# Performance work log

Hardware: AMD Instinct MI355X
Metric: run time of the kernel (lower is better)

## Reference

```python
import jax, jax.numpy as jnp
import numpy as np

SIGMA_BOOST = 2.0   # sparse-hyper util.SIGMA_BOOST
EPSILON = 1e-6      # sparse-hyper util.EPSILON (10e-7)
B, N = 512, 16384   # batch, size


def setup_inputs() -> dict:
    key = jax.random.key(0)
    k1, k2, k3, k4, k5 = jax.random.split(key, 5)
    return {
        "x": jax.random.normal(k1, (B, N), jnp.float32),
        "noise": jax.random.normal(k2, (B, N, 2), jnp.float32),
        "pmeans": jax.random.normal(k3, (N, 2), jnp.float32),
        "psigmas": jax.random.normal(k4, (N,), jnp.float32),
        "pvalues": jax.random.normal(k5, (N,), jnp.float32),
    }


def reference(x, noise, pmeans, psigmas, pvalues):
    b, n = x.shape
    s = jnp.float32(n)  # square size (n, n); both dims equal
    # hyper(): transform_means = sigmoid * (size-1); transform_sigmas = (softplus(.+boost)+eps) * size
    means = jax.nn.sigmoid(pmeans)[None] * (s - 1.0)                    # (1, n, 2) -> bcast (b, n, 2)
    sigmas = (jax.nn.softplus(psigmas + SIGMA_BOOST) + EPSILON)[None, :, None] * s  # (1, n, 1)
    # Normal(means, sigmas).sample() -- non-differentiable sample
    samples = jax.lax.stop_gradient(means + sigmas * noise)             # (b, n, 2)
    # round, clamp to [0, n-1]
    indices = jnp.clip(jnp.round(samples).astype(jnp.int32), 0, n - 1)  # (b, n, 2)
    rows, cols = indices[..., 0], indices[..., 1]                       # (b, n) each
    values = jnp.broadcast_to(pvalues[None, :], (b, n))
    # sparse.contract: y[b, rows[b,t]] += values[b,t] * x[b, cols[b,t]]
    contrib = values * jnp.take_along_axis(x, cols, axis=1)             # (b, n)
    y = jnp.zeros((b, n), x.dtype).at[jnp.arange(b)[:, None], rows].add(contrib)
    return y
```

## Files before the change

kernel.cpp:

```cpp
#include <hip/hip_runtime.h>
#include <math.h>

#define SIGMA_BOOST 2.0f
#define EPSILON 1e-6f

typedef float vfloat4 __attribute__((ext_vector_type(4)));

#define PIN4(v)  asm volatile("" : "+v"(v))
#define PIN1(v)  asm volatile("" : "+v"(v))

__global__ void params_kernel(const float2* __restrict__ pmeans,
                              const float* __restrict__ psigmas,
                              const float* __restrict__ pvalues,
                              float4* __restrict__ params, int N) {
    int t = blockIdx.x * blockDim.x + threadIdx.x;
    if (t >= N) return;
    float2 pm = pmeans[t];
    float scale = (float)(N - 1);
    float m0 = __fmul_rn(__fdiv_rn(1.0f, __fadd_rn(1.0f, expf(-pm.x))), scale);
    float m1 = __fmul_rn(__fdiv_rn(1.0f, __fadd_rn(1.0f, expf(-pm.y))), scale);
    float z  = __fadd_rn(psigmas[t], SIGMA_BOOST);
    float sp = __fadd_rn(fmaxf(z, 0.0f), log1pf(expf(-fabsf(z))));
    float sg = __fmul_rn(__fadd_rn(sp, EPSILON), (float)N);
    params[t] = make_float4(m0, m1, sg, pvalues[t]);
}

template <bool INLINE_PARAMS>
__launch_bounds__(1024, 8)
__global__ void contract_kernel(const float* __restrict__ x,
                                const float2* __restrict__ noise,
                                const float4* __restrict__ params,
                                const float2* __restrict__ pmeans,
                                const float* __restrict__ psigmas,
                                const float* __restrict__ pvalues,
                                float* __restrict__ y, int N) {
    extern __shared__ float ly[];
    const int b = blockIdx.x;
    const int tid = threadIdx.x;
    const int nthr = blockDim.x;

    float4* ly4 = (float4*)ly;
    const int n4 = N >> 2;
    for (int i = tid; i < n4; i += nthr) ly4[i] = make_float4(0.f, 0.f, 0.f, 0.f);
    __syncthreads();

    const float* xb = x + (size_t)b * N;
    const float fN1 = (float)(N - 1);
    const int iN1 = N - 1;
    float acc0 = 0.0f, accE = 0.0f;

    const int steps = ((N >> 1) % nthr == 0) ? (N >> 1) / nthr : 0;

    if (!INLINE_PARAMS && steps >= 2) {
        const vfloat4* nb4 = (const vfloat4*)(noise + (size_t)b * N);
        const vfloat4* pp  = (const vfloat4*)params;

        int q = tid;
        vfloat4 nz = __builtin_nontemporal_load(&nb4[q]);
        vfloat4 pa = pp[2 * q];
        vfloat4 pb = pp[2 * q + 1];
        PIN4(nz); PIN4(pa); PIN4(pb);

        for (int s = 0; s < steps; ++s) {
            float s0 = __fadd_rn(pa.x, __fmul_rn(pa.z, nz.x));
            float s1 = __fadd_rn(pa.y, __fmul_rn(pa.z, nz.y));
            float s2 = __fadd_rn(pb.x, __fmul_rn(pb.z, nz.z));
            float s3 = __fadd_rn(pb.y, __fmul_rn(pb.z, nz.w));
            int r0 = (int)fminf(fmaxf(rintf(s0), 0.0f), fN1);
            int c0 = (int)fminf(fmaxf(rintf(s1), 0.0f), fN1);
            int r1 = (int)fminf(fmaxf(rintf(s2), 0.0f), fN1);
            int c1 = (int)fminf(fmaxf(rintf(s3), 0.0f), fN1);
            float w0 = pa.w, w1 = pb.w;
            float xv0 = xb[c0];
            float xv1 = xb[c1];
            PIN1(xv0); PIN1(xv1);

            vfloat4 nzn, pan, pbn;
            bool have_next = (s + 1 < steps);
            if (have_next) {
                int qn = q + nthr;
                nzn = __builtin_nontemporal_load(&nb4[qn]);
                pan = pp[2 * qn];
                pbn = pp[2 * qn + 1];
                PIN4(nzn); PIN4(pan); PIN4(pbn);
                q = qn;
            }

            float ctr0 = __fmul_rn(w0, xv0);
            float ctr1 = __fmul_rn(w1, xv1);
            bool lo0 = (r0 == 0), hi0 = (r0 == iN1);
            bool lo1 = (r1 == 0), hi1 = (r1 == iN1);
            if (!(lo0 | hi0)) atomicAdd(&ly[r0], ctr0);
            if (!(lo1 | hi1)) atomicAdd(&ly[r1], ctr1);
            acc0 = __fadd_rn(acc0, lo0 ? ctr0 : 0.0f);
            accE = __fadd_rn(accE, hi0 ? ctr0 : 0.0f);
            acc0 = __fadd_rn(acc0, lo1 ? ctr1 : 0.0f);
            accE = __fadd_rn(accE, hi1 ? ctr1 : 0.0f);

            if (have_next) { nz = nzn; pa = pan; pb = pbn; }
        }
    } else {
        const float2* nb = noise + (size_t)b * N;
        for (int t = tid; t < N; t += nthr) {
            float4 p;
            if (INLINE_PARAMS) {
                float2 pm = pmeans[t];
                float scale = (float)(N - 1);
                p.x = __fmul_rn(__fdiv_rn(1.0f, __fadd_rn(1.0f, expf(-pm.x))), scale);
                p.y = __fmul_rn(__fdiv_rn(1.0f, __fadd_rn(1.0f, expf(-pm.y))), scale);
                float z  = __fadd_rn(psigmas[t], SIGMA_BOOST);
                float sp = __fadd_rn(fmaxf(z, 0.0f), log1pf(expf(-fabsf(z))));
                p.z = __fmul_rn(__fadd_rn(sp, EPSILON), (float)N);
                p.w = pvalues[t];
            } else {
                p = params[t];
            }
            float2 nz = nb[t];
            float s0 = __fadd_rn(p.x, __fmul_rn(p.z, nz.x));
            float s1 = __fadd_rn(p.y, __fmul_rn(p.z, nz.y));
            int row = (int)fminf(fmaxf(rintf(s0), 0.0f), fN1);
            int col = (int)fminf(fmaxf(rintf(s1), 0.0f), fN1);
            float xv = xb[col];
            float ctr = __fmul_rn(p.w, xv);
            bool lo = (row == 0);
            bool hi = (row == iN1);
            if (!(lo | hi)) atomicAdd(&ly[row], ctr);
            acc0 = __fadd_rn(acc0, lo ? ctr : 0.0f);
            accE = __fadd_rn(accE, hi ? ctr : 0.0f);
        }
    }

    for (int off = 32; off > 0; off >>= 1) {
        acc0 = __fadd_rn(acc0, __shfl_down(acc0, off, 64));
        accE = __fadd_rn(accE, __shfl_down(accE, off, 64));
    }
    if ((tid & 63) == 0) {
        atomicAdd(&ly[0], acc0);
        atomicAdd(&ly[iN1], accE);
    }
    __syncthreads();

    const vfloat4* lv4 = (const vfloat4*)ly;
    vfloat4* yb4 = (vfloat4*)(y + (size_t)b * N);
    for (int i = tid; i < n4; i += nthr)
        __builtin_nontemporal_store(lv4[i], &yb4[i]);
}

extern "C" void kernel_launch(void* const* d_in, const int* in_sizes, int n_in,
                              void* d_out, int out_size, void* d_ws, size_t ws_size,
                              hipStream_t stream) {
    const float*  x       = (const float*)d_in[0];
    const float2* noise   = (const float2*)d_in[1];
    const float2* pmeans  = (const float2*)d_in[2];
    const float*  psigmas = (const float*)d_in[3];
    const float*  pvalues = (const float*)d_in[4];
    float* y = (float*)d_out;

    const int N = in_sizes[3];
    const int B = in_sizes[0] / N;

    const size_t params_bytes = (size_t)N * sizeof(float4);
    const bool use_ws = (ws_size >= params_bytes) && (d_ws != nullptr);

    const int block = 1024;
    const size_t lds_bytes = (size_t)N * sizeof(float);

    if (use_ws) {
        float4* params = (float4*)d_ws;
        params_kernel<<<(N + 255) / 256, 256, 0, stream>>>(pmeans, psigmas,
                                                           pvalues, params, N);
        contract_kernel<false><<<B, block, lds_bytes, stream>>>(
            x, noise, params, nullptr, nullptr, nullptr, y, N);
    } else {
        contract_kernel<true><<<B, block, lds_bytes, stream>>>(
            x, noise, nullptr, pmeans, psigmas, pvalues, y, N);
    }
}
```

Measured before the change: 149.2 us.

## Stage each batch row of x in LDS and gather from shared memory

Each block now loads its full row of x into a second LDS buffer with coalesced vec4 loads while zeroing the accumulator, then does the random column gather from LDS instead of global memory. This targets the uncoalesced, cache-unfriendly global gathers. In exchange it doubles LDS per block to 128KB, which cuts resident blocks per CU (the launch-bounds hint is lowered to match), and adds a serial staging phase before compute. The kernel decides on the fast path from the shape alone, not from whether the larger LDS allocation actually succeeded, so a failed attribute call would read past its shared memory.

```diff
diff --git a/kernel.cpp b/kernel.cpp
--- a/kernel.cpp
+++ b/kernel.cpp
@@ -7,7 +7,6 @@
 typedef float vfloat4 __attribute__((ext_vector_type(4)));
 
 #define PIN4(v)  asm volatile("" : "+v"(v))
-#define PIN1(v)  asm volatile("" : "+v"(v))
 
 __global__ void params_kernel(const float2* __restrict__ pmeans,
                               const float* __restrict__ psigmas,
@@ -26,7 +25,7 @@
 }
 
 template <bool INLINE_PARAMS>
-__launch_bounds__(1024, 8)
+__launch_bounds__(1024, 4)
 __global__ void contract_kernel(const float* __restrict__ x,
                                 const float2* __restrict__ noise,
                                 const float4* __restrict__ params,
@@ -34,24 +33,38 @@
                                 const float* __restrict__ psigmas,
                                 const float* __restrict__ pvalues,
                                 float* __restrict__ y, int N) {
-    extern __shared__ float ly[];
+    extern __shared__ float lds[];
+    float* ly = lds;
+    float* lx = lds + N;
     const int b = blockIdx.x;
     const int tid = threadIdx.x;
     const int nthr = blockDim.x;
 
-    float4* ly4 = (float4*)ly;
-    const int n4 = N >> 2;
-    for (int i = tid; i < n4; i += nthr) ly4[i] = make_float4(0.f, 0.f, 0.f, 0.f);
-    __syncthreads();
-
     const float* xb = x + (size_t)b * N;
     const float fN1 = (float)(N - 1);
     const int iN1 = N - 1;
+    const int n4 = N >> 2;
+
+    const int steps = ((N >> 1) % nthr == 0) ? (N >> 1) / nthr : 0;
+    const bool fast = !INLINE_PARAMS && steps >= 2 && ((N & 3) == 0);
+
+    float4* ly4 = (float4*)ly;
+    if (fast) {
+        vfloat4* lx4 = (vfloat4*)lx;
+        const vfloat4* xb4 = (const vfloat4*)xb;
+        for (int i = tid; i < n4; i += nthr) {
+            ly4[i] = make_float4(0.f, 0.f, 0.f, 0.f);
+            lx4[i] = xb4[i];
+        }
+    } else {
+        for (int i = tid; i < n4; i += nthr)
+            ly4[i] = make_float4(0.f, 0.f, 0.f, 0.f);
+    }
+    __syncthreads();
+
     float acc0 = 0.0f, accE = 0.0f;
 
-    const int steps = ((N >> 1) % nthr == 0) ? (N >> 1) / nthr : 0;
-
-    if (!INLINE_PARAMS && steps >= 2) {
+    if (fast) {
         const vfloat4* nb4 = (const vfloat4*)(noise + (size_t)b * N);
         const vfloat4* pp  = (const vfloat4*)params;
 
@@ -71,9 +84,8 @@
             int r1 = (int)fminf(fmaxf(rintf(s2), 0.0f), fN1);
             int c1 = (int)fminf(fmaxf(rintf(s3), 0.0f), fN1);
             float w0 = pa.w, w1 = pb.w;
-            float xv0 = xb[c0];
-            float xv1 = xb[c1];
-            PIN1(xv0); PIN1(xv1);
+            float xv0 = lx[c0];
+            float xv1 = lx[c1];
 
             vfloat4 nzn, pan, pbn;
             bool have_next = (s + 1 < steps);
@@ -163,16 +175,28 @@
     const bool use_ws = (ws_size >= params_bytes) && (d_ws != nullptr);
 
     const int block = 1024;
-    const size_t lds_bytes = (size_t)N * sizeof(float);
+    const size_t lds_min  = (size_t)N * sizeof(float);
+    const size_t lds_fast = 2 * lds_min;
+
+    const bool shape_ok = ((N >> 1) % block == 0) && ((N >> 1) / block >= 2) &&
+                          ((N & 3) == 0) && lds_fast <= 160 * 1024;
 
     if (use_ws) {
+        bool fast_ok = shape_ok;
+        if (fast_ok) {
+            hipError_t e = hipFuncSetAttribute(
+                reinterpret_cast<const void*>(&contract_kernel<false>),
+                hipFuncAttributeMaxDynamicSharedMemorySize, (int)lds_fast);
+            fast_ok = (e == hipSuccess);
+        }
         float4* params = (float4*)d_ws;
         params_kernel<<<(N + 255) / 256, 256, 0, stream>>>(pmeans, psigmas,
                                                            pvalues, params, N);
-        contract_kernel<false><<<B, block, lds_bytes, stream>>>(
+        contract_kernel<false><<<B, block,
+                                 fast_ok ? lds_fast : lds_min, stream>>>(
             x, noise, params, nullptr, nullptr, nullptr, y, N);
     } else {
-        contract_kernel<true><<<B, block, lds_bytes, stream>>>(
+        contract_kernel<true><<<B, block, lds_min, stream>>>(
             x, noise, nullptr, pmeans, psigmas, pvalues, y, N);
     }
 }
```

Result: faster. 140.3 us (-5.9%).
